# Optimization experiments

Hardware: AMD Instinct MI355X
Metric: run time of the kernel (lower is better)

## Reference

```python
import jax, jax.numpy as jnp
import numpy as np

HIDDEN = 2048
N_HEADS = 16
HEAD_DIM = HIDDEN // N_HEADS
SEQ = 4096
ROPE_BASE = 10000.0


def setup_inputs() -> dict:
    key = jax.random.key(0)
    ks = jax.random.split(key, 5)
    sc = 1.0 / np.sqrt(HIDDEN)
    return {
        "hidden_states": jax.random.normal(ks[0], (SEQ, HIDDEN), jnp.float32),
        "Wq": jax.random.normal(ks[1], (HIDDEN, HIDDEN), jnp.float32) * sc,
        "Wk": jax.random.normal(ks[2], (HIDDEN, HIDDEN), jnp.float32) * sc,
        "Wv": jax.random.normal(ks[3], (HIDDEN, HIDDEN), jnp.float32) * sc,
        "Wo": jax.random.normal(ks[4], (HIDDEN, HIDDEN), jnp.float32) * sc,
    }


def _rope_cos_sin(seq_len, head_dim, dtype):
    # Llama-style rotary embedding tables, shape [S, 1, head_dim]
    inv_freq = 1.0 / (ROPE_BASE ** (jnp.arange(0, head_dim, 2, dtype=jnp.float32) / head_dim))
    pos = jnp.arange(seq_len, dtype=jnp.float32)
    freqs = pos[:, None] * inv_freq[None, :]          # [S, d/2]
    emb = jnp.concatenate([freqs, freqs], axis=-1)     # [S, d]
    return jnp.cos(emb)[:, None, :].astype(dtype), jnp.sin(emb)[:, None, :].astype(dtype)


def _rotate_half(x):
    h = x.shape[-1] // 2
    return jnp.concatenate([-x[..., h:], x[..., :h]], axis=-1)


def reference(hidden_states, Wq, Wk, Wv, Wo):
    S, H = hidden_states.shape
    d = HEAD_DIM
    # QKV projections (nn.Linear: x @ W.T), split into heads: [S, nH, d]
    q = (hidden_states @ Wq.T).reshape(S, N_HEADS, d)
    k = (hidden_states @ Wk.T).reshape(S, N_HEADS, d)
    v = (hidden_states @ Wv.T).reshape(S, N_HEADS, d)
    # Per-position RoPE on q and k
    cos, sin = _rope_cos_sin(S, d, q.dtype)
    q = q * cos + _rotate_half(q) * sin
    k = k * cos + _rotate_half(k) * sin
    # Causal scaled-dot-product attention, scores [nH, S, S]
    scores = jnp.einsum("snd,tnd->nst", q, k) / jnp.sqrt(jnp.asarray(d, q.dtype))
    causal = jnp.tril(jnp.ones((S, S), dtype=bool))
    scores = jnp.where(causal[None, :, :], scores, jnp.asarray(-1e30, scores.dtype))
    probs = jax.nn.softmax(scores, axis=-1)
    ctx = jnp.einsum("nst,tnd->snd", probs, v).reshape(S, H)
    return ctx @ Wo.T
```

## Files before the change

kernel.cpp:

```cpp
#include <hip/hip_runtime.h>

#define SEQ 4096
#define HIDDEN 2048
#define NHEADS 16
#define HDIM 128
#define QBLK 128
#define KVB 64

typedef float f32x4 __attribute__((ext_vector_type(4)));
typedef __bf16 bf16x8 __attribute__((ext_vector_type(8)));
typedef unsigned int u32x4 __attribute__((ext_vector_type(4)));
typedef unsigned short u16x8 __attribute__((ext_vector_type(8)));
typedef unsigned short u16;

#define SCL2 0.12751747456918851f
#define RLOG 0.2076205059304601f

__device__ __forceinline__ u16 f2bf(float f) {
  unsigned u = __float_as_uint(f);
  unsigned r = 0x7fffu + ((u >> 16) & 1u);
  return (u16)((u + r) >> 16);
}
__device__ __forceinline__ float bf2f(u16 u) {
  return __uint_as_float(((unsigned)u) << 16);
}
__device__ __forceinline__ unsigned cvtpk(float a, float b) {
  unsigned r;
  asm volatile("v_cvt_pk_bf16_f32 %0, %1, %2" : "=v"(r) : "v"(a), "v"(b));
  return r;
}

__device__ __forceinline__ void gload16(const u16* g, u16* l) {
  __builtin_amdgcn_global_load_lds(
      (const __attribute__((address_space(1))) unsigned int*)g,
      (__attribute__((address_space(3))) unsigned int*)l, 16, 0, 0);
}

__device__ __forceinline__ int cumq(int q) {
  return q < 24 ? (q - 12) * 2 : 24 + (q - 24) * 3;
}

__global__ __launch_bounds__(256) void cvt5(const float* __restrict__ X,
    const float* __restrict__ Wq, const float* __restrict__ Wk,
    const float* __restrict__ Wv, const float* __restrict__ Wo,
    u16* __restrict__ dst) {
  const size_t SH = (size_t)SEQ * HIDDEN, HH = (size_t)HIDDEN * HIDDEN;
  size_t i = ((size_t)blockIdx.x * 256 + threadIdx.x) * 8;
  const float* src; size_t off;
  if (i < SH) { src = X; off = i; }
  else if (i < SH + HH) { src = Wq; off = i - SH; }
  else if (i < SH + 2 * HH) { src = Wk; off = i - SH - HH; }
  else if (i < SH + 3 * HH) { src = Wv; off = i - SH - 2 * HH; }
  else { src = Wo; off = i - SH - 3 * HH; }
  float4 a = *reinterpret_cast<const float4*>(src + off);
  float4 b = *reinterpret_cast<const float4*>(src + off + 4);
  u16x8 o;
  o[0] = f2bf(a.x); o[1] = f2bf(a.y); o[2] = f2bf(a.z); o[3] = f2bf(a.w);
  o[4] = f2bf(b.x); o[5] = f2bf(b.y); o[6] = f2bf(b.z); o[7] = f2bf(b.w);
  *reinterpret_cast<u32x4*>(dst + i) = __builtin_bit_cast(u32x4, o);
}

__global__ __launch_bounds__(256, 3) void gemm_qkv(const u16* __restrict__ Xb,
    const u16* __restrict__ Wqb, const u16* __restrict__ Wkb,
    const u16* __restrict__ Wvb, u16* __restrict__ Qo, u16* __restrict__ Ko,
    u16* __restrict__ Vt) {
  __shared__ u16 As[3][4096];
  __shared__ u16 Bs[3][4096];
  const int wg = blockIdx.x;
  const int swz = (wg & 7) * 192 + (wg >> 3);
  const int z = swz >> 9;
  const int rr_ = swz & 511;
  const u16 *A, *B;
  u16* C;
  int bm, bn, cst;
  if (z == 2) {
    A = Wvb; B = Xb; C = Vt;
    bm = (rr_ & 15) << 7; bn = (rr_ >> 4) << 7; cst = SEQ;
  } else {
    A = Xb; B = z ? Wkb : Wqb; C = z ? Ko : Qo;
    bm = (rr_ & 31) << 7; bn = (rr_ >> 5) << 7; cst = HIDDEN;
  }
  const int t = threadIdx.x, lane = t & 63, wave = t >> 6;
  const int lrow = lane & 15, lk = (lane >> 4) * 8;
  const int wr = wave * 32;
  const int r0 = t >> 2, c0 = (t & 3) * 8;

  f32x4 acc[2][8] = {};

  const u16* Ab = A + (size_t)(bm + r0) * HIDDEN + c0;
  const u16* Bb = B + (size_t)(bn + r0) * HIDDEN + c0;
  const size_t rstep = (size_t)64 * HIDDEN;

#define QKV_STAGE(tt, s)                                            \
  {                                                                 \
    const int ko = (tt) * 32;                                       \
    gload16(Ab + ko, &As[s][t * 8]);                                \
    gload16(Bb + ko, &Bs[s][t * 8]);                                \
    gload16(Ab + rstep + ko, &As[s][2048 + t * 8]);                 \
    gload16(Bb + rstep + ko, &Bs[s][2048 + t * 8]);                 \
  }

  QKV_STAGE(0, 0);
  QKV_STAGE(1, 1);
  asm volatile("s_waitcnt vmcnt(4)" ::: "memory");
  __builtin_amdgcn_s_barrier();
  asm volatile("" ::: "memory");

  int sa = 0, sb = 1, sc = 2;
  for (int tt = 0; tt < 64; ++tt) {
    if (tt + 2 < 64) QKV_STAGE(tt + 2, sc);
    bf16x8 af[2], bfv[8];
#pragma unroll
    for (int m = 0; m < 2; ++m)
      af[m] = __builtin_bit_cast(bf16x8,
          *reinterpret_cast<const u32x4*>(&As[sa][(wr + m * 16 + lrow) * 32 + lk]));
#pragma unroll
    for (int n = 0; n < 8; ++n)
      bfv[n] = __builtin_bit_cast(bf16x8,
          *reinterpret_cast<const u32x4*>(&Bs[sa][(n * 16 + lrow) * 32 + lk]));
#pragma unroll
    for (int n = 0; n < 8; ++n)
#pragma unroll
      for (int m = 0; m < 2; ++m)
        acc[m][n] = __builtin_amdgcn_mfma_f32_16x16x32_bf16(af[m], bfv[n], acc[m][n], 0, 0, 0);
    asm volatile("s_waitcnt vmcnt(4)" ::: "memory");
    __builtin_amdgcn_sched_barrier(0);
    __builtin_amdgcn_s_barrier();
    asm volatile("" ::: "memory");
    int s_ = sa; sa = sb; sb = sc; sc = s_;
  }
#undef QKV_STAGE

  const int rb = (lane >> 4) * 4;
  if (z < 2) {
    const float qscale = (z == 0) ? SCL2 : 1.0f;
#pragma unroll
    for (int m = 0; m < 2; ++m)
#pragma unroll
      for (int q = 0; q < 4; ++q) {
        const int s = bm + wr + m * 16 + rb + q;
#pragma unroll
        for (int n = 0; n < 4; ++n) {
          const int ii = n * 16 + lrow;
          float inv = exp2f((float)ii * -RLOG);
          float ang = (float)s * inv;
          float sn, cs;
          __sincosf(ang, &sn, &cs);
          sn *= qscale; cs *= qscale;
          float x1 = acc[m][n][q], x2 = acc[m][n + 4][q];
          acc[m][n][q] = x1 * cs - x2 * sn;
          acc[m][n + 4][q] = x2 * cs + x1 * sn;
        }
      }
  }
#pragma unroll
  for (int m = 0; m < 2; ++m)
#pragma unroll
    for (int n = 0; n < 8; ++n)
#pragma unroll
      for (int q = 0; q < 4; ++q) {
        int col;
        if (z == 2)
          col = bn + (n >> 2) * 64 + ((n >> 1) & 1) * 32 + (lrow >> 2) * 8 +
                (n & 1) * 4 + (lrow & 3);
        else
          col = bn + n * 16 + lrow;
        C[(size_t)(bm + wr + m * 16 + rb + q) * cst + col] = f2bf(acc[m][n][q]);
      }
}

__global__ __launch_bounds__(256, 3) void gemm_out(const u16* __restrict__ A,
    const u16* __restrict__ B, float* __restrict__ C) {
  __shared__ u16 As[3][4096];
  __shared__ u16 Bs[3][4096];
  const int wg = blockIdx.x;
  const int swz = (wg & 7) * 64 + (wg >> 3);
  const int bm = (swz & 31) << 7;
  const int bn = (swz >> 5) << 7;
  const int t = threadIdx.x, lane = t & 63, wave = t >> 6;
  const int lrow = lane & 15, lk = (lane >> 4) * 8;
  const int wr = wave * 32;
  const int r0 = t >> 2, c0 = (t & 3) * 8;

  f32x4 acc[2][8] = {};

  const u16* Ab = A + (size_t)(bm + r0) * HIDDEN + c0;
  const u16* Bb = B + (size_t)(bn + r0) * HIDDEN + c0;
  const size_t rstep = (size_t)64 * HIDDEN;

#define OUT_STAGE(tt, s)                                            \
  {                                                                 \
    const int ko = (tt) * 32;                                       \
    gload16(Ab + ko, &As[s][t * 8]);                                \
    gload16(Bb + ko, &Bs[s][t * 8]);                                \
    gload16(Ab + rstep + ko, &As[s][2048 + t * 8]);                 \
    gload16(Bb + rstep + ko, &Bs[s][2048 + t * 8]);                 \
  }

  OUT_STAGE(0, 0);
  OUT_STAGE(1, 1);
  asm volatile("s_waitcnt vmcnt(4)" ::: "memory");
  __builtin_amdgcn_s_barrier();
  asm volatile("" ::: "memory");

  int sa = 0, sb = 1, sc = 2;
  for (int tt = 0; tt < 64; ++tt) {
    if (tt + 2 < 64) OUT_STAGE(tt + 2, sc);
    bf16x8 af[2], bfv[8];
#pragma unroll
    for (int m = 0; m < 2; ++m)
      af[m] = __builtin_bit_cast(bf16x8,
          *reinterpret_cast<const u32x4*>(&As[sa][(wr + m * 16 + lrow) * 32 + lk]));
#pragma unroll
    for (int n = 0; n < 8; ++n)
      bfv[n] = __builtin_bit_cast(bf16x8,
          *reinterpret_cast<const u32x4*>(&Bs[sa][(n * 16 + lrow) * 32 + lk]));
#pragma unroll
    for (int n = 0; n < 8; ++n)
#pragma unroll
      for (int m = 0; m < 2; ++m)
        acc[m][n] = __builtin_amdgcn_mfma_f32_16x16x32_bf16(af[m], bfv[n], acc[m][n], 0, 0, 0);
    asm volatile("s_waitcnt vmcnt(4)" ::: "memory");
    __builtin_amdgcn_sched_barrier(0);
    __builtin_amdgcn_s_barrier();
    asm volatile("" ::: "memory");
    int s_ = sa; sa = sb; sb = sc; sc = s_;
  }
#undef OUT_STAGE

  const int rb = (lane >> 4) * 4;
#pragma unroll
  for (int m = 0; m < 2; ++m)
#pragma unroll
    for (int n = 0; n < 8; ++n)
#pragma unroll
      for (int q = 0; q < 4; ++q)
        C[(size_t)(bm + wr + m * 16 + rb + q) * HIDDEN + bn + n * 16 + lrow] =
            acc[m][n][q];
}

__global__ __launch_bounds__(512, 4) void attn_kernel(const u16* __restrict__ Q,
                                                      const u16* __restrict__ Kg,
                                                      const u16* __restrict__ Vt,
                                                      u16* __restrict__ O,
                                                      u16* __restrict__ Opart,
                                                      float* __restrict__ Ml) {
  __shared__ u16 Ks[2][KVB * 128];
  __shared__ u16 Vs[2][128 * KVB];
  const int t = threadIdx.x;
  const int wave = t >> 6;
  const int lane = t & 63;
  const int lrow = lane & 15;
  const int lgrp = lane >> 4;

  const int g = blockIdx.x;
  const int h = g & 15;
  const int e = g >> 4;
  int q, c, nc;
  if (e < 24)      { q = 24 + e / 3;           c = e % 3;         nc = 3; }
  else if (e < 48) { q = 23 - ((e - 24) >> 1); c = (e - 24) & 1;  nc = 2; }
  else             { q = 59 - e;               c = 0;             nc = 1; }
  const int total = 2 * q + 2;
  const int base = total / nc, rem = total - base * nc;
  const int it0 = c * base + (c < rem ? c : rem);
  const int it1 = it0 + base + (c < rem ? 1 : 0);

  const int qw = q * QBLK + wave * 16;

  bf16x8 qf[4];
#pragma unroll
  for (int kk = 0; kk < 4; ++kk)
    qf[kk] = __builtin_bit_cast(bf16x8, *reinterpret_cast<const u32x4*>(
        Q + (size_t)(qw + lrow) * HIDDEN + h * HDIM + kk * 32 + lgrp * 8));

  u16x8 ow;
#pragma unroll
  for (int j = 0; j < 8; ++j) ow[j] = (lrow == 0) ? 0x3F80 : 0;
  const bf16x8 vones = __builtin_bit_cast(bf16x8, ow);

  const u16* kgb[2]; const u16* vgb[2]; int kof[2], vof[2];
#pragma unroll
  for (int is = 0; is < 2; ++is) {
    int ch = is * 512 + t;
    int krow = ch >> 4, kslot = ch & 15;
    int kcol = ((kslot & 8) | ((kslot ^ krow) & 7)) * 8;
    kgb[is] = Kg + (size_t)krow * HIDDEN + h * HDIM + kcol;
    kof[is] = ch * 8;
    int vrow = ch >> 3, vslot = ch & 7;
    int vcol = ((vslot ^ vrow) & 7) * 8;
    vgb[is] = Vt + (size_t)(h * HDIM + vrow) * SEQ + vcol;
    vof[is] = ch * 8;
  }

  f32x4 acc[8] = {};
  f32x4 acc1 = {};
  float m2 = -1e30f;

#pragma unroll
  for (int is = 0; is < 2; ++is) {
    gload16(kgb[is] + (size_t)(it0 * KVB) * HIDDEN, &Ks[0][kof[is]]);
    gload16(vgb[is] + it0 * KVB, &Vs[0][vof[is]]);
  }
  __syncthreads();

  int p = 0;
  for (int bt = it0; bt < it1; ++bt) {
    const int t0 = bt * KVB;
    if (bt + 1 < it1) {
      const int t1 = (bt + 1) * KVB;
#pragma unroll
      for (int is = 0; is < 2; ++is) {
        gload16(kgb[is] + (size_t)t1 * HIDDEN, &Ks[p ^ 1][kof[is]]);
        gload16(vgb[is] + t1, &Vs[p ^ 1][vof[is]]);
      }
    }

    if (t0 <= qw + 15) {
      const bool need_mask = (t0 + KVB - 1 > qw);
      f32x4 sc[4] = {};
      __builtin_amdgcn_s_setprio(1);
#pragma unroll
      for (int kk = 0; kk < 4; ++kk) {
#pragma unroll
        for (int colf = 0; colf < 4; ++colf) {
          int trow = colf * 16 + lrow;
          int slot = kk * 4 + lgrp;
          bf16x8 kf = __builtin_bit_cast(bf16x8, *reinterpret_cast<const u32x4*>(
              &Ks[p][trow * 128 + ((slot & 8) | ((slot ^ trow) & 7)) * 8]));
          sc[colf] = __builtin_amdgcn_mfma_f32_16x16x32_bf16(kf, qf[kk], sc[colf], 0, 0, 0);
        }
      }
      __builtin_amdgcn_s_setprio(0);

      const int qg = qw + lrow;
      if (need_mask) {
#pragma unroll
        for (int colf = 0; colf < 4; ++colf) {
          const int kvb0 = t0 + colf * 16 + lgrp * 4;
#pragma unroll
          for (int r = 0; r < 4; ++r)
            sc[colf][r] = (kvb0 + r <= qg) ? sc[colf][r] : -1e30f;
        }
      }
      float mc[4];
#pragma unroll
      for (int colf = 0; colf < 4; ++colf)
        mc[colf] = fmaxf(fmaxf(sc[colf][0], sc[colf][1]),
                         fmaxf(sc[colf][2], sc[colf][3]));
      float mx = fmaxf(fmaxf(mc[0], mc[1]), fmaxf(mc[2], mc[3]));
      mx = fmaxf(mx, __shfl_xor(mx, 16));
      mx = fmaxf(mx, __shfl_xor(mx, 32));

      if (__any(mx > m2 + 11.5f)) {
        float mn = fmaxf(m2, mx);
        float sf = exp2f(m2 - mn);
        m2 = mn;
#pragma unroll
        for (int r = 0; r < 4; ++r) {
          float sfr = __shfl(sf, (lane & 48) | (lgrp * 4 + r));
#pragma unroll
          for (int nn = 0; nn < 8; ++nn) acc[nn][r] *= sfr;
          acc1[r] *= sfr;
        }
      }

      unsigned paw[2][4];
#pragma unroll
      for (int colf = 0; colf < 4; ++colf) {
        float pv[4];
#pragma unroll
        for (int r = 0; r < 4; ++r) pv[r] = exp2f(sc[colf][r] - m2);
        paw[colf >> 1][(colf & 1) * 2 + 0] = cvtpk(pv[0], pv[1]);
        paw[colf >> 1][(colf & 1) * 2 + 1] = cvtpk(pv[2], pv[3]);
      }

      __builtin_amdgcn_s_setprio(1);
#pragma unroll
      for (int ks = 0; ks < 2; ++ks) {
        u32x4 w = {paw[ks][0], paw[ks][1], paw[ks][2], paw[ks][3]};
        bf16x8 pa = __builtin_bit_cast(bf16x8, w);
#pragma unroll
        for (int nn = 0; nn < 8; ++nn) {
          const int d = nn * 16 + lrow;
          bf16x8 vb = __builtin_bit_cast(bf16x8, *reinterpret_cast<const u32x4*>(
              &Vs[p][d * 64 + (((ks * 4 + lgrp) ^ d) & 7) * 8]));
          acc[nn] = __builtin_amdgcn_mfma_f32_16x16x32_bf16(pa, vb, acc[nn], 0, 0, 0);
        }
        acc1 = __builtin_amdgcn_mfma_f32_16x16x32_bf16(pa, vones, acc1, 0, 0, 0);
      }
      __builtin_amdgcn_s_setprio(0);
    }

    __syncthreads();
    p ^= 1;
  }

  if (nc == 1) {
    float inv[4];
#pragma unroll
    for (int r = 0; r < 4; ++r)
      inv[r] = 1.0f / __shfl(acc1[r], lane & 48);
#pragma unroll
    for (int nn = 0; nn < 8; ++nn)
#pragma unroll
      for (int r = 0; r < 4; ++r) {
        int row = qw + lgrp * 4 + r;
        int col = h * HDIM + nn * 16 + lrow;
        O[(size_t)row * HIDDEN + col] = f2bf(acc[nn][r] * inv[r]);
      }
  } else {
    const int slot = h * 48 + cumq(q) + c;
    u16* Op = Opart + (size_t)slot * (QBLK * HDIM);
    float* ml = Ml + (size_t)slot * 256;
#pragma unroll
    for (int nn = 0; nn < 8; ++nn)
#pragma unroll
      for (int r = 0; r < 4; ++r) {
        int rl = wave * 16 + lgrp * 4 + r;
        Op[rl * HDIM + nn * 16 + lrow] = f2bf(acc[nn][r]);
      }
    if (lgrp == 0) {
      int rl = wave * 16 + lrow;
      ml[rl] = m2;
    }
    if (lrow == 0) {
#pragma unroll
      for (int r = 0; r < 4; ++r)
        ml[128 + wave * 16 + lgrp * 4 + r] = acc1[r];
    }
  }
}

__global__ __launch_bounds__(256) void combine_kernel(const u16* __restrict__ Opart,
                                                      const float* __restrict__ Ml,
                                                      u16* __restrict__ O) {
  const int bid = blockIdx.x;
  const int h = bid / 20;
  const int q = 12 + bid % 20;
  const int nc = (q < 24) ? 2 : 3;
  const int sbase = h * 48 + cumq(q);
  const int r = threadIdx.x >> 1;
  const int d0 = (threadIdx.x & 1) * 64;

  float w[3], l = 0.f, M = -3.0e38f;
#pragma unroll
  for (int c = 0; c < 3; ++c)
    if (c < nc) M = fmaxf(M, Ml[(size_t)(sbase + c) * 256 + r]);
#pragma unroll
  for (int c = 0; c < 3; ++c)
    if (c < nc) {
      w[c] = exp2f(Ml[(size_t)(sbase + c) * 256 + r] - M);
      l += w[c] * Ml[(size_t)(sbase + c) * 256 + 128 + r];
    }
  const float inv = 1.0f / l;

  for (int dd = 0; dd < 64; dd += 8) {
    float a8[8] = {};
#pragma unroll
    for (int c = 0; c < 3; ++c)
      if (c < nc) {
        u16x8 v = *reinterpret_cast<const u16x8*>(
            Opart + (size_t)(sbase + c) * (QBLK * HDIM) + r * HDIM + d0 + dd);
#pragma unroll
        for (int j = 0; j < 8; ++j) a8[j] += w[c] * bf2f(v[j]);
      }
    u16x8 o8;
#pragma unroll
    for (int j = 0; j < 8; ++j) o8[j] = f2bf(a8[j] * inv);
    *reinterpret_cast<u16x8*>(
        &O[(size_t)(q * QBLK + r) * HIDDEN + h * HDIM + d0 + dd]) = o8;
  }
}

extern "C" void kernel_launch(void* const* d_in, const int* in_sizes, int n_in,
                              void* d_out, int out_size, void* d_ws, size_t ws_size,
                              hipStream_t stream) {
  const float* X  = (const float*)d_in[0];
  const float* Wq = (const float*)d_in[1];
  const float* Wk = (const float*)d_in[2];
  const float* Wv = (const float*)d_in[3];
  const float* Wo = (const float*)d_in[4];
  float* out = (float*)d_out;

  u16* ws = (u16*)d_ws;
  const size_t SH = (size_t)SEQ * HIDDEN;
  const size_t HH = (size_t)HIDDEN * HIDDEN;
  u16* Xb  = ws;
  u16* Wqb = Xb + SH;
  u16* Wkb = Wqb + HH;
  u16* Wvb = Wkb + HH;
  u16* Wob = Wvb + HH;
  u16* Qb  = Wob + HH;
  u16* Kb  = Qb + SH;
  u16* Vtb = Kb + SH;
  u16* Cb  = Vtb + SH;

  u16* Opart = ws;
  float* Ml = (float*)(ws + (size_t)768 * 16384);

  cvt5<<<(int)((SH + 4 * HH) / 2048), 256, 0, stream>>>(X, Wq, Wk, Wv, Wo, ws);

  gemm_qkv<<<1536, 256, 0, stream>>>(Xb, Wqb, Wkb, Wvb, Qb, Kb, Vtb);

  attn_kernel<<<960, 512, 0, stream>>>(Qb, Kb, Vtb, Cb, Opart, Ml);
  combine_kernel<<<320, 256, 0, stream>>>(Opart, Ml, Cb);

  gemm_out<<<512, 256, 0, stream>>>(Cb, Wob, out);
}
```

Measured before the change: 327.0 us.

## Enlarge QKV GEMM tiles to 256x256 with 8 waves and interleaved staging

The QKV projection GEMM moves from 128x128 tiles with 256 threads and a triple-buffered K=32 pipeline to 256x256 tiles with 512 threads, K=64 double buffering and an XOR-swizzled LDS layout. Global loads for the next stage are split into chunks interleaved between four MFMA phases, and s_setprio raises wave priority during the MFMA bursts. The larger tiles raise arithmetic intensity and reduce global traffic per FLOP. In exchange the grid shrinks to 384 blocks, which may fill the CUs less evenly, and register pressure grows with 128 accumulator floats per thread.

```diff
diff --git a/kernel.cpp b/kernel.cpp
--- a/kernel.cpp
+++ b/kernel.cpp
@@ -60,112 +60,175 @@
   *reinterpret_cast<u32x4*>(dst + i) = __builtin_bit_cast(u32x4, o);
 }
 
-__global__ __launch_bounds__(256, 3) void gemm_qkv(const u16* __restrict__ Xb,
+__global__ __launch_bounds__(512, 2) void gemm_qkv(const u16* __restrict__ Xb,
     const u16* __restrict__ Wqb, const u16* __restrict__ Wkb,
     const u16* __restrict__ Wvb, u16* __restrict__ Qo, u16* __restrict__ Ko,
     u16* __restrict__ Vt) {
-  __shared__ u16 As[3][4096];
-  __shared__ u16 Bs[3][4096];
+  __shared__ u16 As[2][256 * 64];
+  __shared__ u16 Bs[2][256 * 64];
   const int wg = blockIdx.x;
-  const int swz = (wg & 7) * 192 + (wg >> 3);
-  const int z = swz >> 9;
-  const int rr_ = swz & 511;
+  const int swz = (wg & 7) * 48 + (wg >> 3);
+  const int z = swz >> 7;
+  const int rr = swz & 127;
   const u16 *A, *B;
   u16* C;
   int bm, bn, cst;
   if (z == 2) {
     A = Wvb; B = Xb; C = Vt;
-    bm = (rr_ & 15) << 7; bn = (rr_ >> 4) << 7; cst = SEQ;
+    bm = (rr & 7) << 8; bn = (rr >> 3) << 8; cst = SEQ;
   } else {
     A = Xb; B = z ? Wkb : Wqb; C = z ? Ko : Qo;
-    bm = (rr_ & 31) << 7; bn = (rr_ >> 5) << 7; cst = HIDDEN;
-  }
-  const int t = threadIdx.x, lane = t & 63, wave = t >> 6;
-  const int lrow = lane & 15, lk = (lane >> 4) * 8;
-  const int wr = wave * 32;
-  const int r0 = t >> 2, c0 = (t & 3) * 8;
-
-  f32x4 acc[2][8] = {};
-
-  const u16* Ab = A + (size_t)(bm + r0) * HIDDEN + c0;
-  const u16* Bb = B + (size_t)(bn + r0) * HIDDEN + c0;
-  const size_t rstep = (size_t)64 * HIDDEN;
-
-#define QKV_STAGE(tt, s)                                            \
-  {                                                                 \
-    const int ko = (tt) * 32;                                       \
-    gload16(Ab + ko, &As[s][t * 8]);                                \
-    gload16(Bb + ko, &Bs[s][t * 8]);                                \
-    gload16(Ab + rstep + ko, &As[s][2048 + t * 8]);                 \
-    gload16(Bb + rstep + ko, &Bs[s][2048 + t * 8]);                 \
-  }
-
-  QKV_STAGE(0, 0);
-  QKV_STAGE(1, 1);
-  asm volatile("s_waitcnt vmcnt(4)" ::: "memory");
+    bm = (rr & 15) << 8; bn = (rr >> 4) << 8; cst = HIDDEN;
+  }
+  const int t = threadIdx.x;
+  const int wave = t >> 6;
+  const int lane = t & 63;
+  const int lrow = lane & 15, lgrp = lane >> 4;
+  const int wm = wave >> 1;
+  const int wn = wave & 1;
+
+  const int srow = t >> 3;
+  const int sslot = (t & 7) ^ (srow & 7);
+  const u16* Ag = A + (size_t)(bm + srow) * HIDDEN + sslot * 8;
+  const u16* Bg = B + (size_t)(bn + srow) * HIDDEN + sslot * 8;
+  const int dst = t * 8;
+
+  f32x4 acc[4][8] = {};
+
+#define STG_A(R0, kt, s) gload16(Ag + (size_t)(R0) * HIDDEN + (kt), &As[s][(R0) * 64 + dst])
+#define STG_B(R0, kt, s) gload16(Bg + (size_t)(R0) * HIDDEN + (kt), &Bs[s][(R0) * 64 + dst])
+#define LDA(s, row, ks) __builtin_bit_cast(bf16x8, *reinterpret_cast<const u32x4*>( \
+    &As[s][(row) * 64 + (((ks) ^ ((row) & 7)) * 8)]))
+#define LDB(s, row, ks) __builtin_bit_cast(bf16x8, *reinterpret_cast<const u32x4*>( \
+    &Bs[s][(row) * 64 + (((ks) ^ ((row) & 7)) * 8)]))
+
+  STG_A(0, 0, 0); STG_A(64, 0, 0); STG_A(128, 0, 0); STG_A(192, 0, 0);
+  STG_B(0, 0, 0); STG_B(64, 0, 0); STG_B(128, 0, 0); STG_B(192, 0, 0);
+  STG_B(0, 64, 1); STG_B(128, 64, 1);
+  asm volatile("s_waitcnt vmcnt(2)" ::: "memory");
   __builtin_amdgcn_s_barrier();
   asm volatile("" ::: "memory");
 
-  int sa = 0, sb = 1, sc = 2;
-  for (int tt = 0; tt < 64; ++tt) {
-    if (tt + 2 < 64) QKV_STAGE(tt + 2, sc);
-    bf16x8 af[2], bfv[8];
-#pragma unroll
-    for (int m = 0; m < 2; ++m)
-      af[m] = __builtin_bit_cast(bf16x8,
-          *reinterpret_cast<const u32x4*>(&As[sa][(wr + m * 16 + lrow) * 32 + lk]));
-#pragma unroll
-    for (int n = 0; n < 8; ++n)
-      bfv[n] = __builtin_bit_cast(bf16x8,
-          *reinterpret_cast<const u32x4*>(&Bs[sa][(n * 16 + lrow) * 32 + lk]));
-#pragma unroll
-    for (int n = 0; n < 8; ++n)
-#pragma unroll
-      for (int m = 0; m < 2; ++m)
-        acc[m][n] = __builtin_amdgcn_mfma_f32_16x16x32_bf16(af[m], bfv[n], acc[m][n], 0, 0, 0);
-    asm volatile("s_waitcnt vmcnt(4)" ::: "memory");
+  const int arow0 = wm * 64 + lrow;
+  const int brow0 = wn * 128 + lrow;
+
+  for (int tau = 0; tau < 32; ++tau) {
+    const int cur = tau & 1, nxt = cur ^ 1;
+    const int ktn = (tau + 1) * 64;
+    bf16x8 af[4], bfv[4];
+
+#pragma unroll
+    for (int mf = 0; mf < 4; ++mf) af[mf] = LDA(cur, arow0 + mf * 16, lgrp);
+#pragma unroll
+    for (int nf = 0; nf < 4; ++nf) bfv[nf] = LDB(cur, brow0 + nf * 16, lgrp);
+    if (tau + 1 < 32) { STG_B(64, ktn, nxt); STG_B(192, ktn, nxt); }
+    __builtin_amdgcn_s_barrier();
+    asm volatile("s_waitcnt lgkmcnt(0)" ::: "memory");
     __builtin_amdgcn_sched_barrier(0);
+    __builtin_amdgcn_s_setprio(1);
+#pragma unroll
+    for (int mf = 0; mf < 4; ++mf)
+#pragma unroll
+      for (int nf = 0; nf < 4; ++nf)
+        acc[mf][nf] = __builtin_amdgcn_mfma_f32_16x16x32_bf16(af[mf], bfv[nf], acc[mf][nf], 0, 0, 0);
+    __builtin_amdgcn_s_setprio(0);
+    __builtin_amdgcn_s_barrier();
+
+#pragma unroll
+    for (int nf = 0; nf < 4; ++nf) bfv[nf] = LDB(cur, brow0 + (nf + 4) * 16, lgrp);
+    if (tau + 1 < 32) { STG_A(0, ktn, nxt); STG_A(64, ktn, nxt); }
+    __builtin_amdgcn_s_barrier();
+    asm volatile("s_waitcnt lgkmcnt(0)" ::: "memory");
+    __builtin_amdgcn_sched_barrier(0);
+    __builtin_amdgcn_s_setprio(1);
+#pragma unroll
+    for (int mf = 0; mf < 4; ++mf)
+#pragma unroll
+      for (int nf = 0; nf < 4; ++nf)
+        acc[mf][nf + 4] = __builtin_amdgcn_mfma_f32_16x16x32_bf16(af[mf], bfv[nf], acc[mf][nf + 4], 0, 0, 0);
+    __builtin_amdgcn_s_setprio(0);
+    __builtin_amdgcn_s_barrier();
+
+#pragma unroll
+    for (int mf = 0; mf < 4; ++mf) af[mf] = LDA(cur, arow0 + mf * 16, 4 + lgrp);
+#pragma unroll
+    for (int nf = 0; nf < 4; ++nf) bfv[nf] = LDB(cur, brow0 + nf * 16, 4 + lgrp);
+    if (tau + 1 < 32) { STG_A(128, ktn, nxt); STG_A(192, ktn, nxt); }
+    __builtin_amdgcn_s_barrier();
+    asm volatile("s_waitcnt lgkmcnt(0)" ::: "memory");
+    __builtin_amdgcn_sched_barrier(0);
+    __builtin_amdgcn_s_setprio(1);
+#pragma unroll
+    for (int mf = 0; mf < 4; ++mf)
+#pragma unroll
+      for (int nf = 0; nf < 4; ++nf)
+        acc[mf][nf] = __builtin_amdgcn_mfma_f32_16x16x32_bf16(af[mf], bfv[nf], acc[mf][nf], 0, 0, 0);
+    __builtin_amdgcn_s_setprio(0);
+    __builtin_amdgcn_s_barrier();
+
+#pragma unroll
+    for (int nf = 0; nf < 4; ++nf) bfv[nf] = LDB(cur, brow0 + (nf + 4) * 16, 4 + lgrp);
+    if (tau + 2 < 32) { STG_B(0, ktn + 64, cur); STG_B(128, ktn + 64, cur); }
+    __builtin_amdgcn_s_barrier();
+    asm volatile("s_waitcnt lgkmcnt(0)" ::: "memory");
+    __builtin_amdgcn_sched_barrier(0);
+    __builtin_amdgcn_s_setprio(1);
+#pragma unroll
+    for (int mf = 0; mf < 4; ++mf)
+#pragma unroll
+      for (int nf = 0; nf < 4; ++nf)
+        acc[mf][nf + 4] = __builtin_amdgcn_mfma_f32_16x16x32_bf16(af[mf], bfv[nf], acc[mf][nf + 4], 0, 0, 0);
+    __builtin_amdgcn_s_setprio(0);
+    if (tau < 30) {
+      asm volatile("s_waitcnt vmcnt(2)" ::: "memory");
+    } else if (tau == 30) {
+      asm volatile("s_waitcnt vmcnt(0)" ::: "memory");
+    }
+    __builtin_amdgcn_sched_barrier(0);
     __builtin_amdgcn_s_barrier();
     asm volatile("" ::: "memory");
-    int s_ = sa; sa = sb; sb = sc; sc = s_;
-  }
-#undef QKV_STAGE
-
-  const int rb = (lane >> 4) * 4;
+  }
+#undef STG_A
+#undef STG_B
+#undef LDA
+#undef LDB
+
+  const int rbase = lgrp * 4;
   if (z < 2) {
     const float qscale = (z == 0) ? SCL2 : 1.0f;
 #pragma unroll
-    for (int m = 0; m < 2; ++m)
-#pragma unroll
-      for (int q = 0; q < 4; ++q) {
-        const int s = bm + wr + m * 16 + rb + q;
-#pragma unroll
-        for (int n = 0; n < 4; ++n) {
-          const int ii = n * 16 + lrow;
+    for (int mf = 0; mf < 4; ++mf)
+#pragma unroll
+      for (int qq = 0; qq < 4; ++qq) {
+        const int s = bm + wm * 64 + mf * 16 + rbase + qq;
+#pragma unroll
+        for (int nf = 0; nf < 4; ++nf) {
+          const int ii = nf * 16 + lrow;
           float inv = exp2f((float)ii * -RLOG);
           float ang = (float)s * inv;
           float sn, cs;
           __sincosf(ang, &sn, &cs);
           sn *= qscale; cs *= qscale;
-          float x1 = acc[m][n][q], x2 = acc[m][n + 4][q];
-          acc[m][n][q] = x1 * cs - x2 * sn;
-          acc[m][n + 4][q] = x2 * cs + x1 * sn;
+          float x1 = acc[mf][nf][qq], x2 = acc[mf][nf + 4][qq];
+          acc[mf][nf][qq] = x1 * cs - x2 * sn;
+          acc[mf][nf + 4][qq] = x2 * cs + x1 * sn;
         }
       }
   }
 #pragma unroll
-  for (int m = 0; m < 2; ++m)
-#pragma unroll
-    for (int n = 0; n < 8; ++n)
-#pragma unroll
-      for (int q = 0; q < 4; ++q) {
+  for (int mf = 0; mf < 4; ++mf)
+#pragma unroll
+    for (int nf = 0; nf < 8; ++nf)
+#pragma unroll
+      for (int qq = 0; qq < 4; ++qq) {
         int col;
         if (z == 2)
-          col = bn + (n >> 2) * 64 + ((n >> 1) & 1) * 32 + (lrow >> 2) * 8 +
-                (n & 1) * 4 + (lrow & 3);
+          col = bn + wn * 128 + (nf >> 2) * 64 + ((nf >> 1) & 1) * 32 +
+                (lrow >> 2) * 8 + (nf & 1) * 4 + (lrow & 3);
         else
-          col = bn + n * 16 + lrow;
-        C[(size_t)(bm + wr + m * 16 + rb + q) * cst + col] = f2bf(acc[m][n][q]);
+          col = bn + wn * 128 + nf * 16 + lrow;
+        C[(size_t)(bm + wm * 64 + mf * 16 + rbase + qq) * cst + col] =
+            f2bf(acc[mf][nf][qq]);
       }
 }
 
@@ -500,7 +563,7 @@
 
   cvt5<<<(int)((SH + 4 * HH) / 2048), 256, 0, stream>>>(X, Wq, Wk, Wv, Wo, ws);
 
-  gemm_qkv<<<1536, 256, 0, stream>>>(Xb, Wqb, Wkb, Wvb, Qb, Kb, Vtb);
+  gemm_qkv<<<384, 512, 0, stream>>>(Xb, Wqb, Wkb, Wvb, Qb, Kb, Vtb);
 
   attn_kernel<<<960, 512, 0, stream>>>(Qb, Kb, Vtb, Cb, Opart, Ml);
   combine_kernel<<<320, 256, 0, stream>>>(Opart, Ml, Cb);
```

Result: slower. 336.0 us (+2.7%).
